# Optimization experiments

Measured on AMD Instinct MI355X. Metric: run time of the kernel, lower is better.

Reference implementation:

```python
import jax, jax.numpy as jnp
import numpy as np

N, K, D = 8192, 128, 512

def setup_inputs() -> dict:
    key = jax.random.key(0)
    kx, kc = jax.random.split(key)
    x = jax.random.normal(kx, (N, D), dtype=jnp.float32)
    centroids = jax.random.normal(kc, (K, D), dtype=jnp.float32)
    return {"x": x, "centroids": centroids}

def reference(x, centroids):
    # Faithful to torch: dist = (x[:,None,:] - centroids[None]).norm(2, dim=2)
    # Broadcast subtract -> [N, K, D] intermediate, then L2 reduction over D.
    diff = x[:, None, :] - centroids[None, :, :]          # [N, K, D]
    dist = jnp.sqrt(jnp.sum(diff * diff, axis=2))         # [N, K]
    return dist
```

## Files before the change

### kernel.cpp

```cpp
#include <hip/hip_runtime.h>
#include <hip/hip_bf16.h>

#define N_ROWS 8192
#define K_CENT 128
#define D_DIM  512
#define LDS_PITCH 520

typedef short v8s __attribute__((ext_vector_type(8)));
typedef unsigned short v8u __attribute__((ext_vector_type(8)));
typedef float v4f __attribute__((ext_vector_type(4)));

__device__ inline unsigned short f2bf(float f) {
    union { float f; unsigned u; } v; v.f = f;
    unsigned r = v.u + 0x7FFFu + ((v.u >> 16) & 1u);
    return (unsigned short)(r >> 16);
}

__global__ __launch_bounds__(256) void prep_centroids(const float* __restrict__ c,
                                                      float* __restrict__ cnorm,
                                                      unsigned short* __restrict__ cb) {
    int wave = (int)((blockIdx.x * blockDim.x + threadIdx.x) >> 6);
    int lane = threadIdx.x & 63;
    if (wave >= K_CENT) return;
    const float* src = c + (size_t)wave * D_DIM;
    float4 a = ((const float4*)src)[lane];
    float4 b = ((const float4*)src)[64 + lane];
    float s = a.x*a.x + a.y*a.y + a.z*a.z + a.w*a.w
            + b.x*b.x + b.y*b.y + b.z*b.z + b.w*b.w;
    #pragma unroll
    for (int off = 32; off >= 1; off >>= 1) s += __shfl_xor(s, off, 64);
    if (lane == 0) cnorm[wave] = s;
    unsigned short* dst = cb + (size_t)wave * D_DIM;
    ushort4 p0, p1;
    p0.x = f2bf(a.x); p0.y = f2bf(a.y); p0.z = f2bf(a.z); p0.w = f2bf(a.w);
    p1.x = f2bf(b.x); p1.y = f2bf(b.y); p1.z = f2bf(b.z); p1.w = f2bf(b.w);
    ((ushort4*)dst)[lane]      = p0;
    ((ushort4*)dst)[64 + lane] = p1;
}

__global__ __launch_bounds__(512, 4) void dist_kernel(const float* __restrict__ x,
                                                      const unsigned short* __restrict__ cb,
                                                      const float* __restrict__ cnorm,
                                                      float* __restrict__ out) {
    __shared__ unsigned short xlds[16 * LDS_PITCH];

    const int t    = threadIdx.x;
    const int lane = t & 63;
    const int g    = t >> 6;
    const int rowbase = blockIdx.x * 16;

    const float* xs = x + (size_t)rowbase * D_DIM;
    #pragma unroll
    for (int j = 0; j < 2; ++j) {
        int base = j * 4096 + t * 8;
        float4 v0 = *(const float4*)(xs + base);
        float4 v1 = *(const float4*)(xs + base + 4);
        int row = base >> 9;
        int k   = base & 511;
        v8u p;
        p[0] = f2bf(v0.x); p[1] = f2bf(v0.y); p[2] = f2bf(v0.z); p[3] = f2bf(v0.w);
        p[4] = f2bf(v1.x); p[5] = f2bf(v1.y); p[6] = f2bf(v1.z); p[7] = f2bf(v1.w);
        *(v8u*)&xlds[row * LDS_PITCH + k] = p;
    }
    __syncthreads();

    const int n16  = lane & 15;
    const int quad = lane >> 4;
    const unsigned short* bptr = cb + (size_t)(g * 16 + n16) * D_DIM + quad * 8;
    const unsigned short* aptr = &xlds[n16 * LDS_PITCH + quad * 8];

    v4f acc  = (v4f){0.f, 0.f, 0.f, 0.f};
    v4f accx = (v4f){0.f, 0.f, 0.f, 0.f};
    #pragma unroll
    for (int i = 0; i < 16; ++i) {
        v8s af = *(const v8s*)(aptr + i * 32);
        v8s bf = *(const v8s*)(bptr + i * 32);
        acc  = __builtin_amdgcn_mfma_f32_16x16x32_bf16(af, bf, acc, 0, 0, 0);
        accx = __builtin_amdgcn_mfma_f32_16x16x32_bf16(af, af, accx, 0, 0, 0);
    }

    const float cn = cnorm[g * 16 + n16];
    #pragma unroll
    for (int r = 0; r < 4; ++r) {
        float xn = __shfl(accx[r], 20 * quad + r, 64);
        int row = rowbase + quad * 4 + r;
        float d2 = xn + cn - 2.0f * acc[r];
        d2 = d2 > 0.f ? d2 : 0.f;
        out[(size_t)row * K_CENT + g * 16 + n16] = sqrtf(d2);
    }
}

__global__ void naive_kernel(const float* __restrict__ x, const float* __restrict__ c,
                             float* __restrict__ out) {
    int idx = blockIdx.x * blockDim.x + threadIdx.x;
    if (idx >= N_ROWS * K_CENT) return;
    int n = idx / K_CENT, k = idx % K_CENT;
    const float* xr = x + (size_t)n * D_DIM;
    const float* cr = c + (size_t)k * D_DIM;
    float s = 0.f;
    for (int d = 0; d < D_DIM; ++d) { float df = xr[d] - cr[d]; s += df * df; }
    out[idx] = sqrtf(s);
}

extern "C" void kernel_launch(void* const* d_in, const int* in_sizes, int n_in,
                              void* d_out, int out_size, void* d_ws, size_t ws_size,
                              hipStream_t stream) {
    const float* x = (const float*)d_in[0];
    const float* c = (const float*)d_in[1];
    float* out = (float*)d_out;

    const size_t need = 512 + (size_t)K_CENT * D_DIM * sizeof(unsigned short);
    if (ws_size < need) {
        int total = N_ROWS * K_CENT;
        naive_kernel<<<(total + 255) / 256, 256, 0, stream>>>(x, c, out);
        return;
    }

    float* cnorm = (float*)d_ws;
    unsigned short* cb = (unsigned short*)((char*)d_ws + 512);

    prep_centroids<<<(K_CENT * 64 + 255) / 256, 256, 0, stream>>>(c, cnorm, cb);
    dist_kernel<<<N_ROWS / 16, 512, 0, stream>>>(x, cb, cnorm, out);
}
```

Before: 73.76 us.

## Fuse centroid prep into distance kernel with register-resident centroids and double-buffered x tiles

Removes the separate centroid-prep kernel. Each block now converts its centroid slice from fp32 to bf16 with the packed hardware convert instruction, computes centroid norms in registers, and keeps the B fragments in registers across two 16-row tiles. X row norms are computed exactly in fp32 via shuffles instead of an extra MFMA. The second tile's global load is issued before computing the first, to overlap. This saves one launch and the workspace round-trip, but every block re-reads and re-converts the full centroid matrix, and register pressure rises.

```diff
diff --git a/kernel.cpp b/kernel.cpp
--- a/kernel.cpp
+++ b/kernel.cpp
@@ -1,5 +1,4 @@
 #include <hip/hip_runtime.h>
-#include <hip/hip_bf16.h>
 
 #define N_ROWS 8192
 #define K_CENT 128
@@ -7,118 +6,121 @@
 #define LDS_PITCH 520
 
 typedef short v8s __attribute__((ext_vector_type(8)));
-typedef unsigned short v8u __attribute__((ext_vector_type(8)));
 typedef float v4f __attribute__((ext_vector_type(4)));
 
-__device__ inline unsigned short f2bf(float f) {
-    union { float f; unsigned u; } v; v.f = f;
-    unsigned r = v.u + 0x7FFFu + ((v.u >> 16) & 1u);
-    return (unsigned short)(r >> 16);
+union U16B { v8s v; unsigned u[4]; };
+
+__device__ inline unsigned cvt2bf(float lo, float hi) {
+    unsigned r;
+    asm("v_cvt_pk_bf16_f32 %0, %1, %2" : "=v"(r) : "v"(lo), "v"(hi));
+    return r;
 }
 
-__global__ __launch_bounds__(256) void prep_centroids(const float* __restrict__ c,
-                                                      float* __restrict__ cnorm,
-                                                      unsigned short* __restrict__ cb) {
-    int wave = (int)((blockIdx.x * blockDim.x + threadIdx.x) >> 6);
-    int lane = threadIdx.x & 63;
-    if (wave >= K_CENT) return;
-    const float* src = c + (size_t)wave * D_DIM;
-    float4 a = ((const float4*)src)[lane];
-    float4 b = ((const float4*)src)[64 + lane];
-    float s = a.x*a.x + a.y*a.y + a.z*a.z + a.w*a.w
-            + b.x*b.x + b.y*b.y + b.z*b.z + b.w*b.w;
-    #pragma unroll
-    for (int off = 32; off >= 1; off >>= 1) s += __shfl_xor(s, off, 64);
-    if (lane == 0) cnorm[wave] = s;
-    unsigned short* dst = cb + (size_t)wave * D_DIM;
-    ushort4 p0, p1;
-    p0.x = f2bf(a.x); p0.y = f2bf(a.y); p0.z = f2bf(a.z); p0.w = f2bf(a.w);
-    p1.x = f2bf(b.x); p1.y = f2bf(b.y); p1.z = f2bf(b.z); p1.w = f2bf(b.w);
-    ((ushort4*)dst)[lane]      = p0;
-    ((ushort4*)dst)[64 + lane] = p1;
-}
-
-__global__ __launch_bounds__(512, 4) void dist_kernel(const float* __restrict__ x,
-                                                      const unsigned short* __restrict__ cb,
-                                                      const float* __restrict__ cnorm,
-                                                      float* __restrict__ out) {
-    __shared__ unsigned short xlds[16 * LDS_PITCH];
+__global__ __launch_bounds__(512, 2) void dist_fused(const float* __restrict__ x,
+                                                     const float* __restrict__ c,
+                                                     float* __restrict__ out) {
+    __shared__ unsigned short xlds[2][16 * LDS_PITCH];
+    __shared__ __align__(16) float xn[2][16];
 
     const int t    = threadIdx.x;
     const int lane = t & 63;
     const int g    = t >> 6;
-    const int rowbase = blockIdx.x * 16;
+    const int n16  = lane & 15;
+    const int quad = lane >> 4;
+    const int rowbase = blockIdx.x * 32;
 
-    const float* xs = x + (size_t)rowbase * D_DIM;
-    #pragma unroll
-    for (int j = 0; j < 2; ++j) {
-        int base = j * 4096 + t * 8;
-        float4 v0 = *(const float4*)(xs + base);
-        float4 v1 = *(const float4*)(xs + base + 4);
-        int row = base >> 9;
-        int k   = base & 511;
-        v8u p;
-        p[0] = f2bf(v0.x); p[1] = f2bf(v0.y); p[2] = f2bf(v0.z); p[3] = f2bf(v0.w);
-        p[4] = f2bf(v1.x); p[5] = f2bf(v1.y); p[6] = f2bf(v1.z); p[7] = f2bf(v1.w);
-        *(v8u*)&xlds[row * LDS_PITCH + k] = p;
+    const float* xs0 = x + (size_t)rowbase * D_DIM;
+    const float* xs1 = xs0 + 16 * D_DIM;
+
+    float4 a00 = *(const float4*)(xs0 + t * 8);
+    float4 a01 = *(const float4*)(xs0 + t * 8 + 4);
+    float4 a10 = *(const float4*)(xs0 + 4096 + t * 8);
+    float4 a11 = *(const float4*)(xs0 + 4096 + t * 8 + 4);
+
+    const float* cp = c + (size_t)(g * 16 + n16) * D_DIM + quad * 8;
+    v8s bfr[16];
+    float cn0 = 0.f, cn1 = 0.f, cn2 = 0.f, cn3 = 0.f;
+#pragma unroll
+    for (int i = 0; i < 16; ++i) {
+        float4 u0 = *(const float4*)(cp + i * 32);
+        float4 u1 = *(const float4*)(cp + i * 32 + 4);
+        U16B b;
+        b.u[0] = cvt2bf(u0.x, u0.y); b.u[1] = cvt2bf(u0.z, u0.w);
+        b.u[2] = cvt2bf(u1.x, u1.y); b.u[3] = cvt2bf(u1.z, u1.w);
+        bfr[i] = b.v;
+        cn0 += u0.x * u0.x + u0.y * u0.y;
+        cn1 += u0.z * u0.z + u0.w * u0.w;
+        cn2 += u1.x * u1.x + u1.y * u1.y;
+        cn3 += u1.z * u1.z + u1.w * u1.w;
     }
+    float cn = (cn0 + cn1) + (cn2 + cn3);
+    cn += __shfl_xor(cn, 16, 64);
+    cn += __shfl_xor(cn, 32, 64);
+
+    auto stage = [&](int buf, float4 v00, float4 v01, float4 v10, float4 v11) {
+        U16B p0, p1;
+        p0.u[0] = cvt2bf(v00.x, v00.y); p0.u[1] = cvt2bf(v00.z, v00.w);
+        p0.u[2] = cvt2bf(v01.x, v01.y); p0.u[3] = cvt2bf(v01.z, v01.w);
+        p1.u[0] = cvt2bf(v10.x, v10.y); p1.u[1] = cvt2bf(v10.z, v10.w);
+        p1.u[2] = cvt2bf(v11.x, v11.y); p1.u[3] = cvt2bf(v11.z, v11.w);
+        const int k0 = lane * 8;
+        *(v8s*)&xlds[buf][g * LDS_PITCH + k0]       = p0.v;
+        *(v8s*)&xlds[buf][(8 + g) * LDS_PITCH + k0] = p1.v;
+        float s0 = (v00.x * v00.x + v00.y * v00.y + v00.z * v00.z + v00.w * v00.w)
+                 + (v01.x * v01.x + v01.y * v01.y + v01.z * v01.z + v01.w * v01.w);
+        float s1 = (v10.x * v10.x + v10.y * v10.y + v10.z * v10.z + v10.w * v10.w)
+                 + (v11.x * v11.x + v11.y * v11.y + v11.z * v11.z + v11.w * v11.w);
+#pragma unroll
+        for (int off = 32; off >= 1; off >>= 1) {
+            s0 += __shfl_xor(s0, off, 64);
+            s1 += __shfl_xor(s1, off, 64);
+        }
+        if (lane == 0) { xn[buf][g] = s0; xn[buf][8 + g] = s1; }
+    };
+
+    auto compute = [&](int buf, int tilebase) {
+        const unsigned short* ap = &xlds[buf][n16 * LDS_PITCH + quad * 8];
+        v4f acc0 = (v4f){0.f, 0.f, 0.f, 0.f};
+        v4f acc1 = (v4f){0.f, 0.f, 0.f, 0.f};
+#pragma unroll
+        for (int i = 0; i < 16; i += 2) {
+            v8s af0 = *(const v8s*)(ap + i * 32);
+            v8s af1 = *(const v8s*)(ap + (i + 1) * 32);
+            acc0 = __builtin_amdgcn_mfma_f32_16x16x32_bf16(af0, bfr[i],     acc0, 0, 0, 0);
+            acc1 = __builtin_amdgcn_mfma_f32_16x16x32_bf16(af1, bfr[i + 1], acc1, 0, 0, 0);
+        }
+        v4f acc = acc0 + acc1;
+        float4 xr = *(const float4*)&xn[buf][quad * 4];
+        float xra[4] = {xr.x, xr.y, xr.z, xr.w};
+#pragma unroll
+        for (int r = 0; r < 4; ++r) {
+            int row = tilebase + quad * 4 + r;
+            float d2 = xra[r] + cn - 2.0f * acc[r];
+            d2 = d2 > 0.f ? d2 : 0.f;
+            out[(size_t)row * K_CENT + g * 16 + n16] = sqrtf(d2);
+        }
+    };
+
+    stage(0, a00, a01, a10, a11);
     __syncthreads();
 
-    const int n16  = lane & 15;
-    const int quad = lane >> 4;
-    const unsigned short* bptr = cb + (size_t)(g * 16 + n16) * D_DIM + quad * 8;
-    const unsigned short* aptr = &xlds[n16 * LDS_PITCH + quad * 8];
+    float4 b00 = *(const float4*)(xs1 + t * 8);
+    float4 b01 = *(const float4*)(xs1 + t * 8 + 4);
+    float4 b10 = *(const float4*)(xs1 + 4096 + t * 8);
+    float4 b11 = *(const float4*)(xs1 + 4096 + t * 8 + 4);
 
-    v4f acc  = (v4f){0.f, 0.f, 0.f, 0.f};
-    v4f accx = (v4f){0.f, 0.f, 0.f, 0.f};
-    #pragma unroll
-    for (int i = 0; i < 16; ++i) {
-        v8s af = *(const v8s*)(aptr + i * 32);
-        v8s bf = *(const v8s*)(bptr + i * 32);
-        acc  = __builtin_amdgcn_mfma_f32_16x16x32_bf16(af, bf, acc, 0, 0, 0);
-        accx = __builtin_amdgcn_mfma_f32_16x16x32_bf16(af, af, accx, 0, 0, 0);
-    }
-
-    const float cn = cnorm[g * 16 + n16];
-    #pragma unroll
-    for (int r = 0; r < 4; ++r) {
-        float xn = __shfl(accx[r], 20 * quad + r, 64);
-        int row = rowbase + quad * 4 + r;
-        float d2 = xn + cn - 2.0f * acc[r];
-        d2 = d2 > 0.f ? d2 : 0.f;
-        out[(size_t)row * K_CENT + g * 16 + n16] = sqrtf(d2);
-    }
-}
-
-__global__ void naive_kernel(const float* __restrict__ x, const float* __restrict__ c,
-                             float* __restrict__ out) {
-    int idx = blockIdx.x * blockDim.x + threadIdx.x;
-    if (idx >= N_ROWS * K_CENT) return;
-    int n = idx / K_CENT, k = idx % K_CENT;
-    const float* xr = x + (size_t)n * D_DIM;
-    const float* cr = c + (size_t)k * D_DIM;
-    float s = 0.f;
-    for (int d = 0; d < D_DIM; ++d) { float df = xr[d] - cr[d]; s += df * df; }
-    out[idx] = sqrtf(s);
+    compute(0, rowbase);
+    stage(1, b00, b01, b10, b11);
+    __syncthreads();
+    compute(1, rowbase + 16);
 }
 
 extern "C" void kernel_launch(void* const* d_in, const int* in_sizes, int n_in,
                               void* d_out, int out_size, void* d_ws, size_t ws_size,
                               hipStream_t stream) {
+    (void)in_sizes; (void)n_in; (void)d_ws; (void)ws_size; (void)out_size;
     const float* x = (const float*)d_in[0];
     const float* c = (const float*)d_in[1];
     float* out = (float*)d_out;
-
-    const size_t need = 512 + (size_t)K_CENT * D_DIM * sizeof(unsigned short);
-    if (ws_size < need) {
-        int total = N_ROWS * K_CENT;
-        naive_kernel<<<(total + 255) / 256, 256, 0, stream>>>(x, c, out);
-        return;
-    }
-
-    float* cnorm = (float*)d_ws;
-    unsigned short* cb = (unsigned short*)((char*)d_ws + 512);
-
-    prep_centroids<<<(K_CENT * 64 + 255) / 256, 256, 0, stream>>>(c, cnorm, cb);
-    dist_kernel<<<N_ROWS / 16, 512, 0, stream>>>(x, cb, cnorm, out);
+    dist_fused<<<N_ROWS / 32, 512, 0, stream>>>(x, c, out);
 }
```

Measured after the change: 72.66 us. No clear change (-1.5%).
